# Kernel tuning notes

Measured on AMD Instinct MI355X. Metric: run time of the kernel, lower is better.

Reference implementation:

```python
import jax, jax.numpy as jnp
import numpy as np

N_NODES = 10000
N_EDGES = 640000
D_IN, D_HID, D_OUT = 128, 256, 64


def setup_inputs() -> dict:
    key = jax.random.key(0)
    k = jax.random.split(key, 8)
    h = jax.random.normal(k[0], (N_NODES, D_IN), dtype=jnp.float32)
    w = jax.random.uniform(k[1], (N_EDGES, 1), dtype=jnp.float32)
    src = jax.random.randint(k[2], (N_EDGES,), 0, N_NODES, dtype=jnp.int32)
    dst = jax.random.randint(k[3], (N_EDGES,), 0, N_NODES, dtype=jnp.int32)
    W1 = jax.random.normal(k[4], (2 * D_IN, D_HID), dtype=jnp.float32) * (1.0 / np.sqrt(2 * D_IN))
    b1 = jnp.zeros((D_HID,), dtype=jnp.float32)
    W2 = jax.random.normal(k[5], (2 * D_HID, D_OUT), dtype=jnp.float32) * (1.0 / np.sqrt(2 * D_HID))
    b2 = jnp.zeros((D_OUT,), dtype=jnp.float32)
    return {"h": h, "w": w, "src": src, "dst": dst, "W1": W1, "b1": b1, "W2": W2, "b2": b2}


def _sage_layer(h, w, src, dst, W, b, n_nodes):
    # message: m_e = h[src_e] * w_e  (scalar edge weight broadcast over features)
    m = h[src] * w  # [E, D]
    # mean scatter-reduce over incoming edges per destination node
    s = jax.ops.segment_sum(m, dst, num_segments=n_nodes)          # [N, D]
    deg = jax.ops.segment_sum(jnp.ones((dst.shape[0],), h.dtype), dst, num_segments=n_nodes)
    h_N = jnp.where(deg[:, None] > 0, s / jnp.maximum(deg, 1.0)[:, None], 0.0)
    # concat + linear
    return jnp.concatenate([h, h_N], axis=1) @ W + b


def reference(h, w, src, dst, W1, b1, W2, b2):
    n = h.shape[0]
    x = _sage_layer(h, w, src, dst, W1, b1, n)
    x = jax.nn.relu(x)
    return _sage_layer(x, w, src, dst, W2, b2, n)
```

## Files before the change

### kernel.cpp

```cpp
#include <hip/hip_runtime.h>
#include <hip/hip_fp16.h>


#define NSUB 4
#define CAPS 64
#define FB 2048

typedef _Float16 f16x8 __attribute__((ext_vector_type(8)));
typedef float f32x4 __attribute__((ext_vector_type(4)));

#define ACC8P(acc, q, wt)                                        \
  {                                                              \
    const float2 t0 = __half22float2(*(const __half2*)&(q).x);   \
    const float2 t1 = __half22float2(*(const __half2*)&(q).y);   \
    const float2 t2 = __half22float2(*(const __half2*)&(q).z);   \
    const float2 t3 = __half22float2(*(const __half2*)&(q).w);   \
    (acc)[0] += t0.x * (wt); (acc)[1] += t0.y * (wt);            \
    (acc)[2] += t1.x * (wt); (acc)[3] += t1.y * (wt);            \
    (acc)[4] += t2.x * (wt); (acc)[5] += t2.y * (wt);            \
    (acc)[6] += t3.x * (wt); (acc)[7] += t3.y * (wt);            \
  }


__global__ __launch_bounds__(256) void fill_k(const int* __restrict__ src,
                                              const int* __restrict__ dst,
                                              const float* __restrict__ w,
                                              const float* __restrict__ h,
                                              const float* __restrict__ W1,
                                              const float* __restrict__ W2,
                                              int* __restrict__ cursor,
                                              unsigned int* __restrict__ ebuf,
                                              __half* __restrict__ hh,
                                              __half* __restrict__ W1z,
                                              __half* __restrict__ W2z,
                                              int E, int N, int NH4) {
  if (blockIdx.x < FB) {
    const int grp = blockIdx.x & 7;
    const int bi = blockIdx.x >> 3;
    const int nbg = FB >> 3;
    const int chunk = (N + 7) >> 3;
    const int lo = grp * chunk;
    const int hi = min(N, lo + chunk);
    for (int i = bi * 256 + threadIdx.x; i < E; i += nbg * 256) {
      const int d = dst[i];
      if (d >= lo && d < hi) {
        const int sub = i & (NSUB - 1);
        const int p = atomicAdd(&cursor[d * NSUB + sub], 1);
        if (p < CAPS) {
          const __half hw = __float2half_rn(w[i]);
          ebuf[((size_t)d * CAPS + p) * NSUB + sub] =
              ((unsigned int)src[i] << 16) | (unsigned int)__half_as_ushort(hw);
        }
      }
    }
    return;
  }
  const int t = (blockIdx.x - FB) * 256 + threadIdx.x;
  if (t < NH4) {
    const float4 v = reinterpret_cast<const float4*>(h)[t];
    reinterpret_cast<__half2*>(hh)[2 * t] = __floats2half2_rn(v.x, v.y);
    reinterpret_cast<__half2*>(hh)[2 * t + 1] = __floats2half2_rn(v.z, v.w);
    return;
  }
  const int tw1 = t - NH4;
  if (tw1 < 8192) {
    const int ln = tw1 & 63;
    const int nt = (tw1 >> 6) & 15;
    const int kc = tw1 >> 10;
    const int kbase = kc * 32 + (ln >> 4) * 8;
    const int n = nt * 16 + (ln & 15);
    __half tmp[8];
#pragma unroll
    for (int j = 0; j < 8; ++j)
      tmp[j] = __float2half_rn(W1[(size_t)(kbase + j) * 256 + n]);
    *reinterpret_cast<uint4*>(W1z + (size_t)tw1 * 8) = *reinterpret_cast<uint4*>(tmp);
    return;
  }
  const int tw2 = tw1 - 8192;
  if (tw2 < 4096) {
    const int ln = tw2 & 63;
    const int nt = (tw2 >> 6) & 7;
    const int kc = tw2 >> 9;
    const int kbase = kc * 32 + (ln >> 4) * 8;
    const int np = nt * 16 + (ln & 15);
    __half tmp[8];
#pragma unroll
    for (int j = 0; j < 8; ++j) {
      const int k = kbase + j;
      const float v = (np < 64) ? W2[(size_t)k * 64 + np]
                                : W2[(size_t)(256 + k) * 64 + (np - 64)];
      tmp[j] = __float2half_rn(v);
    }
    *reinterpret_cast<uint4*>(W2z + (size_t)tw2 * 8) = *reinterpret_cast<uint4*>(tmp);
  }
}


__global__ __launch_bounds__(256) void ag1g_k(const __half* __restrict__ hh,
                                              const unsigned int* __restrict__ ebuf,
                                              const int* __restrict__ cnt,
                                              const __half* __restrict__ W1z,
                                              const float* __restrict__ b1,
                                              const __half* __restrict__ W2z,
                                              __half* __restrict__ Z,
                                              float* __restrict__ U, int N) {
  const int chunk = (N + 7) >> 3;
  const int g8 = blockIdx.x & 7;
  const int kb = blockIdx.x >> 3;
  const int locbase = kb * 16;
  const int nbase = g8 * chunk + locbase;
  const int tid = threadIdx.x;
  const int wv = tid >> 6;
  const int lane = tid & 63;
  const int g = lane >> 4;
  const int f = lane & 15;

  __shared__ alignas(16) __half As[16][136];
  __shared__ alignas(16) __half Hs[16][264];
  __shared__ alignas(16) float S[16][132];

  const uint4* __restrict__ H = reinterpret_cast<const uint4*>(hh);

  const int row_in = nbase + (lane & 15);
  const int qoff = (lane >> 4) * 8;
  const int colq = lane & 15;
  const int rowq = (lane >> 4) * 4;
  const __half* __restrict__ Ah = hh + (size_t)row_in * 128;
  f16x8 afp[4];
#pragma unroll
  for (int kc = 0; kc < 4; ++kc)
    afp[kc] = *reinterpret_cast<const f16x8*>(Ah + kc * 32 + qoff);
  float bz[4];
#pragma unroll
  for (int nt = 0; nt < 4; ++nt) bz[nt] = b1[wv * 64 + nt * 16 + colq];

  int mM[4], degv[4];
  unsigned int pk[4][NSUB];
  float a[4][8];
#pragma unroll
  for (int i = 0; i < 4; ++i) {
#pragma unroll
    for (int r = 0; r < 8; ++r) a[i][r] = 0.f;
    const int loc = locbase + wv * 4 + i;
    const int n = g8 * chunk + loc;
    const bool valid = (loc < chunk) && (n < N);
    int m0 = 0, m1 = 0, m2 = 0, m3 = 0;
    uint4 pkv = make_uint4(0u, 0u, 0u, 0u);
    if (valid) {
      const int4 c4 = *reinterpret_cast<const int4*>(cnt + n * NSUB);
      m0 = min(c4.x, CAPS);
      m1 = min(c4.y, CAPS);
      m2 = min(c4.z, CAPS);
      m3 = min(c4.w, CAPS);
      pkv = *reinterpret_cast<const uint4*>(ebuf + ((size_t)n * CAPS + lane) * NSUB);
    }
    pk[i][0] = (lane < m0) ? pkv.x : 0u;
    pk[i][1] = (lane < m1) ? pkv.y : 0u;
    pk[i][2] = (lane < m2) ? pkv.z : 0u;
    pk[i][3] = (lane < m3) ? pkv.w : 0u;
    degv[i] = m0 + m1 + m2 + m3;
    mM[i] = max(max(m0, m1), max(m2, m3));
  }
  const int maxAll = max(max(mM[0], mM[1]), max(mM[2], mM[3]));

  for (int j = 0; j < maxAll; j += 4) {
#pragma unroll
    for (int i = 0; i < 4; ++i) {
      if (j < mM[i]) {
        unsigned int p[NSUB];
#pragma unroll
        for (int s = 0; s < NSUB; ++s) p[s] = __shfl(pk[i][s], j + g);
        uint4 q[NSUB];
#pragma unroll
        for (int s = 0; s < NSUB; ++s) q[s] = H[(size_t)(p[s] >> 16) * 16 + f];
#pragma unroll
        for (int s = 0; s < NSUB; ++s) {
          const float wt = __half2float(__ushort_as_half((unsigned short)p[s]));
          ACC8P(a[i], q[s], wt)
        }
      }
    }
  }
#pragma unroll
  for (int i = 0; i < 4; ++i) {
#pragma unroll
    for (int r = 0; r < 8; ++r) {
      a[i][r] += __shfl_xor(a[i][r], 16);
      a[i][r] += __shfl_xor(a[i][r], 32);
    }
    if (lane < 16) {
      const float inv = (degv[i] > 0) ? 1.0f / (float)degv[i] : 0.0f;
      __half tmp[8];
#pragma unroll
      for (int r = 0; r < 8; ++r) tmp[r] = __float2half_rn(a[i][r] * inv);
      *reinterpret_cast<uint4*>(&As[wv * 4 + i][f * 8]) =
          *reinterpret_cast<uint4*>(tmp);
    }
  }
  __syncthreads();

  const int w = wv;
  f32x4 acc[4] = {};
#pragma unroll
  for (int kc = 0; kc < 8; ++kc) {
    const f16x8 af =
        (kc < 4) ? afp[kc]
                 : *reinterpret_cast<const f16x8*>(&As[lane & 15][(kc - 4) * 32 + qoff]);
    const __half* bbase = W1z + ((size_t)(kc * 16 + w * 4) * 64 + lane) * 8;
#pragma unroll
    for (int nt = 0; nt < 4; ++nt) {
      const f16x8 bf = *reinterpret_cast<const f16x8*>(bbase + (size_t)nt * 64 * 8);
      acc[nt] = __builtin_amdgcn_mfma_f32_16x16x32_f16(af, bf, acc[nt], 0, 0, 0);
    }
  }
#pragma unroll
  for (int nt = 0; nt < 4; ++nt) {
    const int col = w * 64 + nt * 16 + colq;
#pragma unroll
    for (int r = 0; r < 4; ++r)
      Hs[rowq + r][col] = __float2half_rn(fmaxf(acc[nt][r] + bz[nt], 0.f));
  }
  __syncthreads();

  f32x4 accz[2] = {};
#pragma unroll
  for (int kc = 0; kc < 8; ++kc) {
    const f16x8 af = *reinterpret_cast<const f16x8*>(&Hs[lane & 15][kc * 32 + qoff]);
    const __half* bbase = W2z + ((size_t)(kc * 8 + w * 2) * 64 + lane) * 8;
#pragma unroll
    for (int nt = 0; nt < 2; ++nt) {
      const f16x8 bf = *reinterpret_cast<const f16x8*>(bbase + (size_t)nt * 64 * 8);
      accz[nt] = __builtin_amdgcn_mfma_f32_16x16x32_f16(af, bf, accz[nt], 0, 0, 0);
    }
  }
#pragma unroll
  for (int nt = 0; nt < 2; ++nt) {
    const int col = w * 32 + nt * 16 + colq;
#pragma unroll
    for (int r = 0; r < 4; ++r) S[rowq + r][col] = accz[nt][r];
  }
  __syncthreads();
  {
    const int row = tid >> 4, c4 = tid & 15;
    if (locbase + row < chunk && nbase + row < N) {
      const float4 v = make_float4(S[row][c4 * 4], S[row][c4 * 4 + 1],
                                   S[row][c4 * 4 + 2], S[row][c4 * 4 + 3]);
      *reinterpret_cast<float4*>(&U[(size_t)(nbase + row) * 64 + c4 * 4]) = v;
    }
  }
  if (tid < 128) {
    const int row = tid >> 3, c8 = tid & 7;
    if (locbase + row < chunk && nbase + row < N) {
      const float* s = &S[row][64 + c8 * 8];
      const __half2 h0 = __floats2half2_rn(s[0], s[1]);
      const __half2 h1 = __floats2half2_rn(s[2], s[3]);
      const __half2 h2 = __floats2half2_rn(s[4], s[5]);
      const __half2 h3 = __floats2half2_rn(s[6], s[7]);
      uint4 q;
      q.x = *reinterpret_cast<const unsigned int*>(&h0);
      q.y = *reinterpret_cast<const unsigned int*>(&h1);
      q.z = *reinterpret_cast<const unsigned int*>(&h2);
      q.w = *reinterpret_cast<const unsigned int*>(&h3);
      *reinterpret_cast<uint4*>(&Z[(size_t)(nbase + row) * 64 + c8 * 8]) = q;
    }
  }
}


__global__ __launch_bounds__(256) void agg2z_k(const __half* __restrict__ Z,
                                               const float* __restrict__ U,
                                               const float* __restrict__ b2,
                                               const unsigned int* __restrict__ ebuf,
                                               const int* __restrict__ cnt,
                                               float* __restrict__ out, int N) {
  const int chunk = (N + 7) >> 3;
  const int g8 = blockIdx.x & 7;
  const int k = blockIdx.x >> 3;
  const int loc = k * 4 + (threadIdx.x >> 6);
  const int n = g8 * chunk + loc;
  if (loc >= chunk || n >= N) return;
  const int lane = threadIdx.x & 63;
  const int g = lane >> 3;
  const int f = lane & 7;
  const uint4* __restrict__ Zr = reinterpret_cast<const uint4*>(Z);

  const int4 c4 = *reinterpret_cast<const int4*>(cnt + n * NSUB);
  int m[NSUB];
  m[0] = min(c4.x, CAPS);
  m[1] = min(c4.y, CAPS);
  m[2] = min(c4.z, CAPS);
  m[3] = min(c4.w, CAPS);
  const int deg = m[0] + m[1] + m[2] + m[3];
  const int mMax = max(max(m[0], m[1]), max(m[2], m[3]));

  const uint4 pkv =
      *reinterpret_cast<const uint4*>(ebuf + ((size_t)n * CAPS + lane) * NSUB);
  unsigned int pk[NSUB];
  pk[0] = (lane < m[0]) ? pkv.x : 0u;
  pk[1] = (lane < m[1]) ? pkv.y : 0u;
  pk[2] = (lane < m[2]) ? pkv.z : 0u;
  pk[3] = (lane < m[3]) ? pkv.w : 0u;

  const float4 u0 = *reinterpret_cast<const float4*>(&U[(size_t)n * 64 + f * 8]);
  const float4 u1 = *reinterpret_cast<const float4*>(&U[(size_t)n * 64 + f * 8 + 4]);
  const float4 z0 = *reinterpret_cast<const float4*>(&b2[f * 8]);
  const float4 z1 = *reinterpret_cast<const float4*>(&b2[f * 8 + 4]);

  float a[8] = {};
  for (int j = 0; j < mMax; j += 16) {
    unsigned int pA[NSUB], pB[NSUB];
#pragma unroll
    for (int s = 0; s < NSUB; ++s) {
      pA[s] = __shfl(pk[s], j + g);
      pB[s] = __shfl(pk[s], j + 8 + g);
    }
    uint4 qA[NSUB], qB[NSUB];
#pragma unroll
    for (int s = 0; s < NSUB; ++s) {
      qA[s] = Zr[(size_t)(pA[s] >> 16) * 8 + f];
      qB[s] = Zr[(size_t)(pB[s] >> 16) * 8 + f];
    }
#pragma unroll
    for (int s = 0; s < NSUB; ++s) {
      const float wA = __half2float(__ushort_as_half((unsigned short)pA[s]));
      const float wB = __half2float(__ushort_as_half((unsigned short)pB[s]));
      ACC8P(a, qA[s], wA)
      ACC8P(a, qB[s], wB)
    }
  }
#pragma unroll
  for (int r = 0; r < 8; ++r) {
    a[r] += __shfl_xor(a[r], 8);
    a[r] += __shfl_xor(a[r], 16);
    a[r] += __shfl_xor(a[r], 32);
  }
  if (lane < 8) {
    const float inv = (deg > 0) ? 1.0f / (float)deg : 0.0f;
    float4 o0, o1;
    o0.x = a[0] * inv + u0.x + z0.x;
    o0.y = a[1] * inv + u0.y + z0.y;
    o0.z = a[2] * inv + u0.z + z0.z;
    o0.w = a[3] * inv + u0.w + z0.w;
    o1.x = a[4] * inv + u1.x + z1.x;
    o1.y = a[5] * inv + u1.y + z1.y;
    o1.z = a[6] * inv + u1.z + z1.z;
    o1.w = a[7] * inv + u1.w + z1.w;
    *reinterpret_cast<float4*>(&out[(size_t)n * 64 + f * 8]) = o0;
    *reinterpret_cast<float4*>(&out[(size_t)n * 64 + f * 8 + 4]) = o1;
  }
}


extern "C" void kernel_launch(void* const* d_in, const int* in_sizes, int n_in,
                              void* d_out, int out_size, void* d_ws, size_t ws_size,
                              hipStream_t stream) {
  const float* h   = (const float*)d_in[0];
  const float* w   = (const float*)d_in[1];
  const int*   src = (const int*)d_in[2];
  const int*   dst = (const int*)d_in[3];
  const float* W1  = (const float*)d_in[4];
  const float* b1  = (const float*)d_in[5];
  const float* W2  = (const float*)d_in[6];
  const float* b2  = (const float*)d_in[7];
  float* out = (float*)d_out;

  const int N = in_sizes[0] / 128;
  const int E = in_sizes[2];

  char* ws = (char*)d_ws;
  size_t o = 0;
  auto alloc = [&](size_t bytes) -> void* {
    void* p = ws + o;
    o = (o + bytes + 255) & ~(size_t)255;
    return p;
  };
  int*          cursor = (int*)alloc((size_t)N * NSUB * 4);
  unsigned int* ebuf   = (unsigned int*)alloc((size_t)N * NSUB * CAPS * 4);
  __half*       hh     = (__half*)alloc((size_t)N * 128 * 2);
  __half*       Z      = (__half*)alloc((size_t)N * 64 * 2);
  float*        U      = (float*)alloc((size_t)N * 64 * 4);
  __half*       W1z    = (__half*)alloc((size_t)256 * 256 * 2);
  __half*       W2z    = (__half*)alloc((size_t)256 * 128 * 2);

  const int NH4 = N * 32;
  const int prep_blocks = (NH4 + 8192 + 4096 + 255) / 256;
  const int chunk = (N + 7) >> 3;

  hipMemsetAsync(cursor, 0, (size_t)N * NSUB * 4, stream);
  fill_k<<<FB + prep_blocks, 256, 0, stream>>>(src, dst, w, h, W1, W2, cursor,
                                               ebuf, hh, W1z, W2z, E, N, NH4);
  ag1g_k<<<8 * ((chunk + 15) >> 4), 256, 0, stream>>>(hh, ebuf, cursor, W1z, b1,
                                                      W2z, Z, U, N);
  agg2z_k<<<8 * ((chunk + 3) / 4), 256, 0, stream>>>(Z, U, b2, ebuf, cursor, out, N);
}
```

Baseline: 138.0 us.

## Flatten edge bucketing to one pass and double waves in layer-1 kernel

The bucketing phase of fill_k used to have each of eight block groups scan every edge and keep only those whose destination fell in its node range. It now assigns one edge per thread over a flat grid, so each edge is read once. Separately, ag1g_k moves to 512 threads (8 waves), with each wave gathering 2 nodes instead of 4 and computing half as many MFMA output tiles in both GEMMs. The intent is to cut the eightfold redundant edge reads and to add latency hiding in the gather. The cost is that bucket slot order now follows atomic arrival across the whole grid rather than per group, and the larger blocks may lower occupancy.

```diff
diff --git a/kernel.cpp b/kernel.cpp
--- a/kernel.cpp
+++ b/kernel.cpp
@@ -4,7 +4,6 @@
 
 #define NSUB 4
 #define CAPS 64
-#define FB 2048
 
 typedef _Float16 f16x8 __attribute__((ext_vector_type(8)));
 typedef float f32x4 __attribute__((ext_vector_type(4)));
@@ -33,29 +32,22 @@
                                               __half* __restrict__ hh,
                                               __half* __restrict__ W1z,
                                               __half* __restrict__ W2z,
-                                              int E, int N, int NH4) {
-  if (blockIdx.x < FB) {
-    const int grp = blockIdx.x & 7;
-    const int bi = blockIdx.x >> 3;
-    const int nbg = FB >> 3;
-    const int chunk = (N + 7) >> 3;
-    const int lo = grp * chunk;
-    const int hi = min(N, lo + chunk);
-    for (int i = bi * 256 + threadIdx.x; i < E; i += nbg * 256) {
+                                              int E, int N, int NH4, int EB) {
+  if (blockIdx.x < (unsigned)EB) {
+    const int i = blockIdx.x * 256 + threadIdx.x;
+    if (i < E) {
       const int d = dst[i];
-      if (d >= lo && d < hi) {
-        const int sub = i & (NSUB - 1);
-        const int p = atomicAdd(&cursor[d * NSUB + sub], 1);
-        if (p < CAPS) {
-          const __half hw = __float2half_rn(w[i]);
-          ebuf[((size_t)d * CAPS + p) * NSUB + sub] =
-              ((unsigned int)src[i] << 16) | (unsigned int)__half_as_ushort(hw);
-        }
+      const int sub = i & (NSUB - 1);
+      const int p = atomicAdd(&cursor[d * NSUB + sub], 1);
+      if (p < CAPS) {
+        const __half hw = __float2half_rn(w[i]);
+        ebuf[((size_t)d * CAPS + p) * NSUB + sub] =
+            ((unsigned int)src[i] << 16) | (unsigned int)__half_as_ushort(hw);
       }
     }
     return;
   }
-  const int t = (blockIdx.x - FB) * 256 + threadIdx.x;
+  const int t = (blockIdx.x - EB) * 256 + threadIdx.x;
   if (t < NH4) {
     const float4 v = reinterpret_cast<const float4*>(h)[t];
     reinterpret_cast<__half2*>(hh)[2 * t] = __floats2half2_rn(v.x, v.y);
@@ -96,7 +88,7 @@
 }
 
 
-__global__ __launch_bounds__(256) void ag1g_k(const __half* __restrict__ hh,
+__global__ __launch_bounds__(512) void ag1g_k(const __half* __restrict__ hh,
                                               const unsigned int* __restrict__ ebuf,
                                               const int* __restrict__ cnt,
                                               const __half* __restrict__ W1z,
@@ -130,18 +122,18 @@
 #pragma unroll
   for (int kc = 0; kc < 4; ++kc)
     afp[kc] = *reinterpret_cast<const f16x8*>(Ah + kc * 32 + qoff);
-  float bz[4];
-#pragma unroll
-  for (int nt = 0; nt < 4; ++nt) bz[nt] = b1[wv * 64 + nt * 16 + colq];
-
-  int mM[4], degv[4];
-  unsigned int pk[4][NSUB];
-  float a[4][8];
-#pragma unroll
-  for (int i = 0; i < 4; ++i) {
+  float bz[2];
+#pragma unroll
+  for (int nt = 0; nt < 2; ++nt) bz[nt] = b1[wv * 32 + nt * 16 + colq];
+
+  int mM[2], degv[2];
+  unsigned int pk[2][NSUB];
+  float a[2][8];
+#pragma unroll
+  for (int i = 0; i < 2; ++i) {
 #pragma unroll
     for (int r = 0; r < 8; ++r) a[i][r] = 0.f;
-    const int loc = locbase + wv * 4 + i;
+    const int loc = locbase + wv * 2 + i;
     const int n = g8 * chunk + loc;
     const bool valid = (loc < chunk) && (n < N);
     int m0 = 0, m1 = 0, m2 = 0, m3 = 0;
@@ -161,11 +153,11 @@
     degv[i] = m0 + m1 + m2 + m3;
     mM[i] = max(max(m0, m1), max(m2, m3));
   }
-  const int maxAll = max(max(mM[0], mM[1]), max(mM[2], mM[3]));
+  const int maxAll = max(mM[0], mM[1]);
 
   for (int j = 0; j < maxAll; j += 4) {
 #pragma unroll
-    for (int i = 0; i < 4; ++i) {
+    for (int i = 0; i < 2; ++i) {
       if (j < mM[i]) {
         unsigned int p[NSUB];
 #pragma unroll
@@ -182,7 +174,7 @@
     }
   }
 #pragma unroll
-  for (int i = 0; i < 4; ++i) {
+  for (int i = 0; i < 2; ++i) {
 #pragma unroll
     for (int r = 0; r < 8; ++r) {
       a[i][r] += __shfl_xor(a[i][r], 16);
@@ -193,54 +185,49 @@
       __half tmp[8];
 #pragma unroll
       for (int r = 0; r < 8; ++r) tmp[r] = __float2half_rn(a[i][r] * inv);
-      *reinterpret_cast<uint4*>(&As[wv * 4 + i][f * 8]) =
+      *reinterpret_cast<uint4*>(&As[wv * 2 + i][f * 8]) =
           *reinterpret_cast<uint4*>(tmp);
     }
   }
   __syncthreads();
 
-  const int w = wv;
-  f32x4 acc[4] = {};
+  f32x4 acc[2] = {};
 #pragma unroll
   for (int kc = 0; kc < 8; ++kc) {
     const f16x8 af =
         (kc < 4) ? afp[kc]
                  : *reinterpret_cast<const f16x8*>(&As[lane & 15][(kc - 4) * 32 + qoff]);
-    const __half* bbase = W1z + ((size_t)(kc * 16 + w * 4) * 64 + lane) * 8;
-#pragma unroll
-    for (int nt = 0; nt < 4; ++nt) {
+    const __half* bbase = W1z + ((size_t)(kc * 16 + wv * 2) * 64 + lane) * 8;
+#pragma unroll
+    for (int nt = 0; nt < 2; ++nt) {
       const f16x8 bf = *reinterpret_cast<const f16x8*>(bbase + (size_t)nt * 64 * 8);
       acc[nt] = __builtin_amdgcn_mfma_f32_16x16x32_f16(af, bf, acc[nt], 0, 0, 0);
     }
   }
 #pragma unroll
-  for (int nt = 0; nt < 4; ++nt) {
-    const int col = w * 64 + nt * 16 + colq;
+  for (int nt = 0; nt < 2; ++nt) {
+    const int col = wv * 32 + nt * 16 + colq;
 #pragma unroll
     for (int r = 0; r < 4; ++r)
       Hs[rowq + r][col] = __float2half_rn(fmaxf(acc[nt][r] + bz[nt], 0.f));
   }
   __syncthreads();
 
-  f32x4 accz[2] = {};
+  f32x4 accz = {};
 #pragma unroll
   for (int kc = 0; kc < 8; ++kc) {
     const f16x8 af = *reinterpret_cast<const f16x8*>(&Hs[lane & 15][kc * 32 + qoff]);
-    const __half* bbase = W2z + ((size_t)(kc * 8 + w * 2) * 64 + lane) * 8;
-#pragma unroll
-    for (int nt = 0; nt < 2; ++nt) {
-      const f16x8 bf = *reinterpret_cast<const f16x8*>(bbase + (size_t)nt * 64 * 8);
-      accz[nt] = __builtin_amdgcn_mfma_f32_16x16x32_f16(af, bf, accz[nt], 0, 0, 0);
-    }
-  }
-#pragma unroll
-  for (int nt = 0; nt < 2; ++nt) {
-    const int col = w * 32 + nt * 16 + colq;
-#pragma unroll
-    for (int r = 0; r < 4; ++r) S[rowq + r][col] = accz[nt][r];
+    const f16x8 bf =
+        *reinterpret_cast<const f16x8*>(W2z + ((size_t)(kc * 8 + wv) * 64 + lane) * 8);
+    accz = __builtin_amdgcn_mfma_f32_16x16x32_f16(af, bf, accz, 0, 0, 0);
+  }
+  {
+    const int col = wv * 16 + colq;
+#pragma unroll
+    for (int r = 0; r < 4; ++r) S[rowq + r][col] = accz[r];
   }
   __syncthreads();
-  {
+  if (tid < 256) {
     const int row = tid >> 4, c4 = tid & 15;
     if (locbase + row < chunk && nbase + row < N) {
       const float4 v = make_float4(S[row][c4 * 4], S[row][c4 * 4 + 1],
@@ -383,13 +370,14 @@
   __half*       W2z    = (__half*)alloc((size_t)256 * 128 * 2);
 
   const int NH4 = N * 32;
+  const int EB = (E + 255) >> 8;
   const int prep_blocks = (NH4 + 8192 + 4096 + 255) / 256;
   const int chunk = (N + 7) >> 3;
 
   hipMemsetAsync(cursor, 0, (size_t)N * NSUB * 4, stream);
-  fill_k<<<FB + prep_blocks, 256, 0, stream>>>(src, dst, w, h, W1, W2, cursor,
-                                               ebuf, hh, W1z, W2z, E, N, NH4);
-  ag1g_k<<<8 * ((chunk + 15) >> 4), 256, 0, stream>>>(hh, ebuf, cursor, W1z, b1,
+  fill_k<<<EB + prep_blocks, 256, 0, stream>>>(src, dst, w, h, W1, W2, cursor,
+                                               ebuf, hh, W1z, W2z, E, N, NH4, EB);
+  ag1g_k<<<8 * ((chunk + 15) >> 4), 512, 0, stream>>>(hh, ebuf, cursor, W1z, b1,
                                                       W2z, Z, U, N);
   agg2z_k<<<8 * ((chunk + 3) / 4), 256, 0, stream>>>(Z, U, b2, ebuf, cursor, out, N);
 }
```

New measurement: 139.6 us. No clear change (+1.2%).
